# Optimization experiments

Measured on AMD Instinct MI355X. Metric: run time of the kernel, lower is better.

Reference implementation:

```python
import jax, jax.numpy as jnp
import numpy as np
import math

MAX_K = 8
MAX_LEN = 128
ITER = 3
GAMMA = 2
NEG = -2.0**16 + 1.0  # mask fill value from torch code


def _squash(x):
    # NOTE: faithful to source: norm taken over axis=1 (capsule axis), keepdim
    sq = jnp.sum(x * x, axis=1, keepdims=True)
    return sq / (1.0 + sq) / jnp.sqrt(sq + 1e-9) * x


def _routing(low, B_mat, S):
    # low: [B, n, d] mailbox; B_mat: [1, MAX_K, MAX_LEN]; S: [d, d]
    n = low.shape[1]
    K_c = max(1, min(MAX_K, int(math.log2(n))))  # static per edge type
    low_new = jnp.einsum('bnd,de->bne', low, S)  # loop-invariant in torch too
    B_c = B_mat[:, :K_c, :]
    mask = jnp.arange(MAX_LEN) < n  # padded-neighbor mask
    high = None
    for _ in range(ITER):
        logits = jnp.where(mask, B_c, NEG)              # [1,K_c,L]
        W = jax.nn.softmax(logits, axis=-1)[:, :, :n]   # weights identical over batch
        high = _squash(jnp.einsum('xkn,bnd->bkd', W, low_new))
        delta = jnp.einsum('bkd,bnd->kn', high, low_new)  # batch-summed agreement
        B_c = B_c.at[0, :, :n].add(delta)  # padded cols get zero delta (zeros in low)
    high = jnp.pad(high, ((0, 0), (0, MAX_K - K_c), (0, 0)))
    # torch B_matrix_c aliases B_matrix; write slice back so next etype sees updates
    return high, B_mat.at[:, :K_c, :].set(B_c)


def setup_inputs() -> dict:
    key = jax.random.key(0)
    ks = jax.random.split(key, 12)
    d = 64
    n_user, n_rev, n_tag, n_rev_dst = 10000, 30000, 40000, 8000
    f = lambda k, s: jax.random.normal(k, s, dtype=jnp.float32)
    return {
        'review_embed': f(ks[0], (n_rev, d)),
        'tag_embed': f(ks[1], (n_tag, d)),
        'idx_urt': jax.random.randint(ks[2], (n_user, 64), 0, n_rev, dtype=jnp.int32),
        'idx_uqt': jax.random.randint(ks[3], (n_user, 32), 0, n_tag, dtype=jnp.int32),
        'idx_uprt': jax.random.randint(ks[4], (n_user, 50), 0, n_rev, dtype=jnp.int32),
        'idx_rht': jax.random.randint(ks[5], (n_rev_dst, 20), 0, n_tag, dtype=jnp.int32),
        'B_matrix': f(ks[6], (1, MAX_K, MAX_LEN)),
        'S_matrix': f(ks[7], (d, d)),
        'M1': f(ks[8], (d, d)),
        'M2': f(ks[9], (d, 1)),
    }


def reference(review_embed, tag_embed, idx_urt, idx_uqt, idx_uprt, idx_rht,
              B_matrix, S_matrix, M1, M2):
    # capsule routing per edge type, B_matrix threaded sequentially (torch aliasing)
    h_urt, B_matrix = _routing(review_embed[idx_urt], B_matrix, S_matrix)
    h_uqt, B_matrix = _routing(tag_embed[idx_uqt], B_matrix, S_matrix)
    h_uprt, B_matrix = _routing(review_embed[idx_uprt], B_matrix, S_matrix)
    all_u = jnp.concatenate([h_urt, h_uqt, h_uprt], axis=1)  # [B, 3*MAX_K, d]
    s = jnp.einsum('bkd,do->bko', jnp.tanh(jnp.einsum('bkd,de->bke', all_u, M1)), M2)[..., 0]
    s = s ** GAMMA
    att = jax.nn.softmax(s, axis=1)                # [B, 3*MAX_K]
    user_out = jnp.einsum('bk,bkd->bd', att, all_u)
    review_out = jnp.mean(tag_embed[idx_rht], axis=1)  # flag==2 mean reduce (r_h_t)
    return user_out, review_out
```

## Files before the change

kernel.cpp:

```cpp
#include <hip/hip_runtime.h>

#define NU 10000
#define NREV_DST 8000
#define MAIN_BLOCKS 2500


__device__ __forceinline__ float rlane(float v, int l) {
    return __int_as_float(__builtin_amdgcn_readlane(__float_as_int(v), l));
}

template <int N, int K>
__global__ __launch_bounds__(256, 4) void main_iter(
    const float* __restrict__ emb, const int* __restrict__ idx,
    const float* __restrict__ Sg, const float* __restrict__ Wg,
    float* __restrict__ delta_acc, float* __restrict__ allu,
    int slot0, int write_high, int write_delta)
{
    __shared__ float s_S[64 * 64];
    __shared__ float s_embT[4][64 * 20];

    const int tid  = threadIdx.x;
    const int w    = tid >> 6;
    const int lane = tid & 63;

    for (int i = tid; i < 64 * 64; i += 256) {
        const int r = i >> 6, c = i & 63;
        s_S[r * 64 + ((((c >> 2) ^ (r & 15)) << 2) | (c & 3))] = Sg[i];
    }
    __syncthreads();

    const int u = __builtin_amdgcn_readfirstlane((int)blockIdx.x * 4 + w);
    const int* uidx = idx + u * N;

    float g[K];
#pragma unroll
    for (int k = 0; k < K; ++k) g[k] = 0.f;
#pragma unroll
    for (int r0 = 0; r0 < N; r0 += 8) {
        float ev[8];
#pragma unroll
        for (int i = 0; i < 8; ++i)
            if (r0 + i < N) {
                const int row = uidx[r0 + i];
                ev[i] = emb[(size_t)row * 64 + lane];
            }
#pragma unroll
        for (int i = 0; i < 8; ++i)
            if (r0 + i < N) {
#pragma unroll
                for (int k = 0; k < K; ++k)
                    g[k] = fmaf(Wg[(r0 + i) * 8 + k], ev[i], g[k]);
            }
    }

    float raw[K];
#pragma unroll
    for (int k = 0; k < K; ++k) raw[k] = 0.f;
    {
        const int l4 = lane >> 2, lo = lane & 3;
#pragma unroll 4
        for (int eo = 0; eo < 16; ++eo) {
            const int a = eo * 64 + (((l4 ^ eo) << 2) | lo);
            const float sv0 = s_S[a];
            const float sv1 = s_S[a + 16 * 64];
            const float sv2 = s_S[a + 32 * 64];
            const float sv3 = s_S[a + 48 * 64];
#pragma unroll
            for (int k = 0; k < K; ++k) {
                raw[k] = fmaf(rlane(g[k], eo),      sv0, raw[k]);
                raw[k] = fmaf(rlane(g[k], eo + 16), sv1, raw[k]);
                raw[k] = fmaf(rlane(g[k], eo + 32), sv2, raw[k]);
                raw[k] = fmaf(rlane(g[k], eo + 48), sv3, raw[k]);
            }
        }
    }

    float sq = 0.f;
#pragma unroll
    for (int k = 0; k < K; ++k) sq = fmaf(raw[k], raw[k], sq);
    const float f = (sq / (1.0f + sq)) / sqrtf(sq + 1e-9f);
    float hi[K];
#pragma unroll
    for (int k = 0; k < K; ++k) hi[k] = f * raw[k];

    if (write_high) {
#pragma unroll
        for (int k = 0; k < K; ++k)
            allu[(size_t)u * 1024 + (slot0 + k) * 64 + lane] = hi[k];
    }

    if (write_delta) {
        float hs[K];
#pragma unroll
        for (int k = 0; k < K; ++k) hs[k] = 0.f;
        {
            const int rowbase = lane * 64, l15 = lane & 15;
#pragma unroll 4
            for (int d4 = 0; d4 < 16; ++d4) {
                const float4 sv = *(const float4*)&s_S[rowbase + ((d4 ^ l15) << 2)];
#pragma unroll
                for (int k = 0; k < K; ++k) {
                    hs[k] = fmaf(rlane(hi[k], d4 * 4 + 0), sv.x, hs[k]);
                    hs[k] = fmaf(rlane(hi[k], d4 * 4 + 1), sv.y, hs[k]);
                    hs[k] = fmaf(rlane(hi[k], d4 * 4 + 2), sv.z, hs[k]);
                    hs[k] = fmaf(rlane(hi[k], d4 * 4 + 3), sv.w, hs[k]);
                }
            }
        }

        float dreg[K];
#pragma unroll
        for (int k = 0; k < K; ++k) dreg[k] = 0.f;

        constexpr int RP = (N + 15) / 16;
        const int rr = lane >> 2, jj = lane & 3;
        int rows[RP];
#pragma unroll
        for (int p = 0; p < RP; ++p) {
            const int r = p * 16 + rr;
            rows[p] = (N % 16 == 0 || r < N) ? uidx[r] : 0;
        }

        for (int ec = 0; ec < 4; ++ec) {
            const int e0 = ec * 16;
#pragma unroll
            for (int p = 0; p < RP; ++p) {
                const int r = p * 16 + rr;
                if (N % 16 == 0 || r < N) {
                    const float4 v =
                        *(const float4*)(emb + (size_t)rows[p] * 64 + e0 + jj * 4);
                    *(float4*)&s_embT[w][r * 20 + jj * 4] = v;
                }
            }
#pragma unroll
            for (int e4 = 0; e4 < 4; ++e4) {
                const float4 v = *(const float4*)&s_embT[w][lane * 20 + e4 * 4];
                const int e = e0 + e4 * 4;
#pragma unroll
                for (int k = 0; k < K; ++k) {
                    dreg[k] = fmaf(v.x, rlane(hs[k], e + 0), dreg[k]);
                    dreg[k] = fmaf(v.y, rlane(hs[k], e + 1), dreg[k]);
                    dreg[k] = fmaf(v.z, rlane(hs[k], e + 2), dreg[k]);
                    dreg[k] = fmaf(v.w, rlane(hs[k], e + 3), dreg[k]);
                }
            }
        }

#pragma unroll
        for (int k = 0; k < K; ++k) s_embT[w][k * 64 + lane] = dreg[k];
        __syncthreads();
        for (int t = tid; t < K * 64; t += 256) {
            const float s = s_embT[0][t] + s_embT[1][t] + s_embT[2][t] + s_embT[3][t];
            if ((t & 63) < N) atomicAdd(&delta_acc[t], s);
        }
    }
}

__global__ __launch_bounds__(1024) void update_kernel(
    float* __restrict__ Bstate, float* __restrict__ delta_acc,
    const float* __restrict__ Bin, float* __restrict__ Wout,
    int init, int Kc, int nc, int Kn, int nn)
{
    __shared__ float sB[1024];
    const int t = threadIdx.x;
    float b = init ? Bin[t] : Bstate[t];
    const int k = t >> 7, n = t & 127;
    float d = 0.f;
    if (!init && k < Kc && n < nc) d = delta_acc[k * 64 + n];
    __syncthreads();
    if (t < 512) delta_acc[t] = 0.f;
    b += d;
    Bstate[t] = b;
    sB[t] = b;
    __syncthreads();
    const int wv = t >> 6, lane = t & 63;
    if (wv < Kn) {
        float v = (lane < nn) ? sB[wv * 128 + lane] : -3.4e38f;
        float m = v;
#pragma unroll
        for (int off = 32; off >= 1; off >>= 1) m = fmaxf(m, __shfl_xor(m, off, 64));
        const float e = (lane < nn) ? expf(v - m) : 0.f;
        float s = e;
#pragma unroll
        for (int off = 32; off >= 1; off >>= 1) s += __shfl_xor(s, off, 64);
        Wout[lane * 8 + wv] = e / s;
    }
}

__global__ __launch_bounds__(256) void attn_kernel(
    const float* __restrict__ allu, const float* __restrict__ M1g,
    const float* __restrict__ M2g, float* __restrict__ out)
{
    __shared__ float sM1[64 * 65];
    __shared__ float sU[4][16 * 64];
    const int tid = threadIdx.x, w = tid >> 6, lane = tid & 63;
    for (int i = tid; i < 4096; i += 256)
        sM1[(i >> 6) * 65 + (i & 63)] = M1g[i];
    __syncthreads();
    const int u = blockIdx.x * 4 + w;
    if (u >= NU) return;
    for (int i = 0; i < 16; ++i)
        sU[w][i * 64 + lane] = allu[(size_t)u * 1024 + i * 64 + lane];
    const float m2 = M2g[lane];
    float acc[16];
#pragma unroll
    for (int i = 0; i < 16; ++i) acc[i] = 0.f;
    for (int d = 0; d < 64; ++d) {
        const float m1v = sM1[d * 65 + lane];
#pragma unroll
        for (int i = 0; i < 16; ++i) acc[i] = fmaf(sU[w][i * 64 + d], m1v, acc[i]);
    }
    float s2[16];
#pragma unroll
    for (int i = 0; i < 16; ++i) {
        float c = tanhf(acc[i]) * m2;
#pragma unroll
        for (int off = 32; off >= 1; off >>= 1) c += __shfl_xor(c, off, 64);
        s2[i] = c * c;
    }
    float mx = 0.f;
#pragma unroll
    for (int i = 0; i < 16; ++i) mx = fmaxf(mx, s2[i]);
    float den = 8.f * expf(-mx);
    float att[16];
#pragma unroll
    for (int i = 0; i < 16; ++i) { att[i] = expf(s2[i] - mx); den += att[i]; }
    const float inv = 1.0f / den;
    float o = 0.f;
#pragma unroll
    for (int i = 0; i < 16; ++i) o = fmaf(att[i] * inv, sU[w][i * 64 + lane], o);
    out[(size_t)u * 64 + lane] = o;
}

__global__ __launch_bounds__(256) void review_kernel(
    const float* __restrict__ tag, const int* __restrict__ idx, float* __restrict__ out)
{
    const int tid = threadIdx.x, w = tid >> 6, lane = tid & 63;
    const int r = blockIdx.x * 4 + w;
    if (r >= NREV_DST) return;
    float acc = 0.f;
    for (int j = 0; j < 20; ++j) {
        const int t = idx[r * 20 + j];
        acc += tag[(size_t)t * 64 + lane];
    }
    out[(size_t)r * 64 + lane] = acc / 20.0f;
}

extern "C" void kernel_launch(void* const* d_in, const int* in_sizes, int n_in,
                              void* d_out, int out_size, void* d_ws, size_t ws_size,
                              hipStream_t stream)
{
    const float* review_embed = (const float*)d_in[0];
    const float* tag_embed    = (const float*)d_in[1];
    const int*   idx_urt      = (const int*)d_in[2];
    const int*   idx_uqt      = (const int*)d_in[3];
    const int*   idx_uprt     = (const int*)d_in[4];
    const int*   idx_rht      = (const int*)d_in[5];
    const float* B_in         = (const float*)d_in[6];
    const float* S_g          = (const float*)d_in[7];
    const float* M1           = (const float*)d_in[8];
    const float* M2           = (const float*)d_in[9];

    float* ws     = (float*)d_ws;
    float* Bstate = ws;
    float* delta  = ws + 1024;
    float* Wbuf   = ws + 1536;
    float* allu   = ws + 2048;
    float* out    = (float*)d_out;

    const dim3 mg(MAIN_BLOCKS), mb(256);
    const dim3 one(1), ub(1024);

    hipLaunchKernelGGL(update_kernel, one, ub, 0, stream,
                       Bstate, delta, B_in, Wbuf, 1, 0, 0, 6, 64);

    for (int itr = 0; itr < 3; ++itr) {
        hipLaunchKernelGGL((main_iter<64, 6>), mg, mb, 0, stream,
                           review_embed, idx_urt, S_g, Wbuf, delta, allu,
                           0, (itr == 2) ? 1 : 0, 1);
        const int Kn = (itr == 2) ? 5 : 6;
        const int nn = (itr == 2) ? 32 : 64;
        hipLaunchKernelGGL(update_kernel, one, ub, 0, stream,
                           Bstate, delta, B_in, Wbuf, 0, 6, 64, Kn, nn);
    }
    for (int itr = 0; itr < 3; ++itr) {
        hipLaunchKernelGGL((main_iter<32, 5>), mg, mb, 0, stream,
                           tag_embed, idx_uqt, S_g, Wbuf, delta, allu,
                           6, (itr == 2) ? 1 : 0, 1);
        const int nn = (itr == 2) ? 50 : 32;
        hipLaunchKernelGGL(update_kernel, one, ub, 0, stream,
                           Bstate, delta, B_in, Wbuf, 0, 5, 32, 5, nn);
    }
    for (int itr = 0; itr < 3; ++itr) {
        const int last = (itr == 2);
        hipLaunchKernelGGL((main_iter<50, 5>), mg, mb, 0, stream,
                           review_embed, idx_uprt, S_g, Wbuf, delta, allu,
                           11, last, last ? 0 : 1);
        if (!last)
            hipLaunchKernelGGL(update_kernel, one, ub, 0, stream,
                               Bstate, delta, B_in, Wbuf, 0, 5, 50, 5, 50);
    }

    hipLaunchKernelGGL(attn_kernel, dim3((NU + 3) / 4), mb, 0, stream, allu, M1, M2, out);
    hipLaunchKernelGGL(review_kernel, dim3((NREV_DST + 3) / 4), mb, 0, stream,
                       tag_embed, idx_rht, out + (size_t)NU * 64);
}
```

Baseline: 793.3 us.

## Precompute embedding-times-S tables and drop in-kernel S matmuls

Adds a kernel that multiplies each embedding table by S once per edge type, so the routing kernels gather pre-transformed rows instead of applying S per user per iteration. The delta step now dots high vectors directly against the transformed rows held in shared memory, replacing the S-projection and readlane broadcasts. This removes the per-block S load into shared memory and most of the FMAs, and raises occupancy hints. In exchange it adds three table-transform launches and extra workspace traffic, and recomputes the review table twice.

```diff
diff --git a/kernel.cpp b/kernel.cpp
--- a/kernel.cpp
+++ b/kernel.cpp
@@ -5,36 +5,46 @@
 #define MAIN_BLOCKS 2500
 
 
-__device__ __forceinline__ float rlane(float v, int l) {
-    return __int_as_float(__builtin_amdgcn_readlane(__float_as_int(v), l));
+__global__ __launch_bounds__(256) void embS_kernel(
+    const float* __restrict__ E, const float* __restrict__ Sg,
+    float* __restrict__ out, int nrows)
+{
+    const int tid = threadIdx.x, w = tid >> 6, lane = tid & 63;
+    float Sc[64];
+#pragma unroll
+    for (int e = 0; e < 64; ++e) Sc[e] = Sg[e * 64 + lane];
+    const int nw = gridDim.x * 4;
+    for (int r0 = blockIdx.x * 4 + w; r0 < nrows; r0 += nw) {
+        const int r = __builtin_amdgcn_readfirstlane(r0);
+        const float* row = E + (size_t)r * 64;
+        float acc = 0.f;
+#pragma unroll
+        for (int e = 0; e < 64; ++e)
+            acc = fmaf(row[e], Sc[e], acc);
+        out[(size_t)r * 64 + lane] = acc;
+    }
 }
 
 template <int N, int K>
-__global__ __launch_bounds__(256, 4) void main_iter(
-    const float* __restrict__ emb, const int* __restrict__ idx,
-    const float* __restrict__ Sg, const float* __restrict__ Wg,
+__global__ __launch_bounds__(256, 6) void main_iter(
+    const float* __restrict__ embS, const int* __restrict__ idx,
+    const float* __restrict__ Wg,
     float* __restrict__ delta_acc, float* __restrict__ allu,
     int slot0, int write_high, int write_delta)
 {
-    __shared__ float s_S[64 * 64];
-    __shared__ float s_embT[4][64 * 20];
+    __shared__ float s_slab[4][64 * 20];
+    __shared__ float s_h[4][K * 64];
 
     const int tid  = threadIdx.x;
     const int w    = tid >> 6;
     const int lane = tid & 63;
 
-    for (int i = tid; i < 64 * 64; i += 256) {
-        const int r = i >> 6, c = i & 63;
-        s_S[r * 64 + ((((c >> 2) ^ (r & 15)) << 2) | (c & 3))] = Sg[i];
-    }
-    __syncthreads();
-
     const int u = __builtin_amdgcn_readfirstlane((int)blockIdx.x * 4 + w);
     const int* uidx = idx + u * N;
 
-    float g[K];
-#pragma unroll
-    for (int k = 0; k < K; ++k) g[k] = 0.f;
+    float raw[K];
+#pragma unroll
+    for (int k = 0; k < K; ++k) raw[k] = 0.f;
 #pragma unroll
     for (int r0 = 0; r0 < N; r0 += 8) {
         float ev[8];
@@ -42,37 +52,15 @@
         for (int i = 0; i < 8; ++i)
             if (r0 + i < N) {
                 const int row = uidx[r0 + i];
-                ev[i] = emb[(size_t)row * 64 + lane];
+                ev[i] = embS[(size_t)row * 64 + lane];
             }
 #pragma unroll
         for (int i = 0; i < 8; ++i)
             if (r0 + i < N) {
 #pragma unroll
                 for (int k = 0; k < K; ++k)
-                    g[k] = fmaf(Wg[(r0 + i) * 8 + k], ev[i], g[k]);
-            }
-    }
-
-    float raw[K];
-#pragma unroll
-    for (int k = 0; k < K; ++k) raw[k] = 0.f;
-    {
-        const int l4 = lane >> 2, lo = lane & 3;
-#pragma unroll 4
-        for (int eo = 0; eo < 16; ++eo) {
-            const int a = eo * 64 + (((l4 ^ eo) << 2) | lo);
-            const float sv0 = s_S[a];
-            const float sv1 = s_S[a + 16 * 64];
-            const float sv2 = s_S[a + 32 * 64];
-            const float sv3 = s_S[a + 48 * 64];
-#pragma unroll
-            for (int k = 0; k < K; ++k) {
-                raw[k] = fmaf(rlane(g[k], eo),      sv0, raw[k]);
-                raw[k] = fmaf(rlane(g[k], eo + 16), sv1, raw[k]);
-                raw[k] = fmaf(rlane(g[k], eo + 32), sv2, raw[k]);
-                raw[k] = fmaf(rlane(g[k], eo + 48), sv3, raw[k]);
-            }
-        }
+                    raw[k] = fmaf(Wg[(r0 + i) * 8 + k], ev[i], raw[k]);
+            }
     }
 
     float sq = 0.f;
@@ -90,23 +78,8 @@
     }
 
     if (write_delta) {
-        float hs[K];
-#pragma unroll
-        for (int k = 0; k < K; ++k) hs[k] = 0.f;
-        {
-            const int rowbase = lane * 64, l15 = lane & 15;
-#pragma unroll 4
-            for (int d4 = 0; d4 < 16; ++d4) {
-                const float4 sv = *(const float4*)&s_S[rowbase + ((d4 ^ l15) << 2)];
-#pragma unroll
-                for (int k = 0; k < K; ++k) {
-                    hs[k] = fmaf(rlane(hi[k], d4 * 4 + 0), sv.x, hs[k]);
-                    hs[k] = fmaf(rlane(hi[k], d4 * 4 + 1), sv.y, hs[k]);
-                    hs[k] = fmaf(rlane(hi[k], d4 * 4 + 2), sv.z, hs[k]);
-                    hs[k] = fmaf(rlane(hi[k], d4 * 4 + 3), sv.w, hs[k]);
-                }
-            }
-        }
+#pragma unroll
+        for (int k = 0; k < K; ++k) s_h[w][k * 64 + lane] = hi[k];
 
         float dreg[K];
 #pragma unroll
@@ -128,29 +101,29 @@
                 const int r = p * 16 + rr;
                 if (N % 16 == 0 || r < N) {
                     const float4 v =
-                        *(const float4*)(emb + (size_t)rows[p] * 64 + e0 + jj * 4);
-                    *(float4*)&s_embT[w][r * 20 + jj * 4] = v;
+                        *(const float4*)(embS + (size_t)rows[p] * 64 + e0 + jj * 4);
+                    *(float4*)&s_slab[w][r * 20 + jj * 4] = v;
                 }
             }
 #pragma unroll
             for (int e4 = 0; e4 < 4; ++e4) {
-                const float4 v = *(const float4*)&s_embT[w][lane * 20 + e4 * 4];
-                const int e = e0 + e4 * 4;
+                const float4 v = *(const float4*)&s_slab[w][lane * 20 + e4 * 4];
 #pragma unroll
                 for (int k = 0; k < K; ++k) {
-                    dreg[k] = fmaf(v.x, rlane(hs[k], e + 0), dreg[k]);
-                    dreg[k] = fmaf(v.y, rlane(hs[k], e + 1), dreg[k]);
-                    dreg[k] = fmaf(v.z, rlane(hs[k], e + 2), dreg[k]);
-                    dreg[k] = fmaf(v.w, rlane(hs[k], e + 3), dreg[k]);
+                    const float4 h = *(const float4*)&s_h[w][k * 64 + e0 + e4 * 4];
+                    dreg[k] = fmaf(v.x, h.x, dreg[k]);
+                    dreg[k] = fmaf(v.y, h.y, dreg[k]);
+                    dreg[k] = fmaf(v.z, h.z, dreg[k]);
+                    dreg[k] = fmaf(v.w, h.w, dreg[k]);
                 }
             }
         }
 
 #pragma unroll
-        for (int k = 0; k < K; ++k) s_embT[w][k * 64 + lane] = dreg[k];
+        for (int k = 0; k < K; ++k) s_slab[w][k * 64 + lane] = dreg[k];
         __syncthreads();
         for (int t = tid; t < K * 64; t += 256) {
-            const float s = s_embT[0][t] + s_embT[1][t] + s_embT[2][t] + s_embT[3][t];
+            const float s = s_slab[0][t] + s_slab[1][t] + s_slab[2][t] + s_slab[3][t];
             if ((t & 63) < N) atomicAdd(&delta_acc[t], s);
         }
     }
@@ -266,35 +239,41 @@
     float* delta  = ws + 1024;
     float* Wbuf   = ws + 1536;
     float* allu   = ws + 2048;
+    float* embS   = ws + 2048 + (size_t)NU * 1024;
     float* out    = (float*)d_out;
 
     const dim3 mg(MAIN_BLOCKS), mb(256);
-    const dim3 one(1), ub(1024);
-
+    const dim3 one(1), ub(1024), pg(512);
+
+    hipLaunchKernelGGL(embS_kernel, pg, mb, 0, stream, review_embed, S_g, embS, 30000);
     hipLaunchKernelGGL(update_kernel, one, ub, 0, stream,
                        Bstate, delta, B_in, Wbuf, 1, 0, 0, 6, 64);
 
     for (int itr = 0; itr < 3; ++itr) {
         hipLaunchKernelGGL((main_iter<64, 6>), mg, mb, 0, stream,
-                           review_embed, idx_urt, S_g, Wbuf, delta, allu,
+                           embS, idx_urt, Wbuf, delta, allu,
                            0, (itr == 2) ? 1 : 0, 1);
         const int Kn = (itr == 2) ? 5 : 6;
         const int nn = (itr == 2) ? 32 : 64;
         hipLaunchKernelGGL(update_kernel, one, ub, 0, stream,
                            Bstate, delta, B_in, Wbuf, 0, 6, 64, Kn, nn);
     }
+
+    hipLaunchKernelGGL(embS_kernel, pg, mb, 0, stream, tag_embed, S_g, embS, 40000);
     for (int itr = 0; itr < 3; ++itr) {
         hipLaunchKernelGGL((main_iter<32, 5>), mg, mb, 0, stream,
-                           tag_embed, idx_uqt, S_g, Wbuf, delta, allu,
+                           embS, idx_uqt, Wbuf, delta, allu,
                            6, (itr == 2) ? 1 : 0, 1);
         const int nn = (itr == 2) ? 50 : 32;
         hipLaunchKernelGGL(update_kernel, one, ub, 0, stream,
                            Bstate, delta, B_in, Wbuf, 0, 5, 32, 5, nn);
     }
+
+    hipLaunchKernelGGL(embS_kernel, pg, mb, 0, stream, review_embed, S_g, embS, 30000);
     for (int itr = 0; itr < 3; ++itr) {
         const int last = (itr == 2);
         hipLaunchKernelGGL((main_iter<50, 5>), mg, mb, 0, stream,
-                           review_embed, idx_uprt, S_g, Wbuf, delta, allu,
+                           embS, idx_uprt, Wbuf, delta, allu,
                            11, last, last ? 0 : 1);
         if (!last)
             hipLaunchKernelGGL(update_kernel, one, ub, 0, stream,
```

Result: slower. 1.134 ms (+42.9%).

## Replace readlane broadcasts with LDS-staged vectors and fuse init with review kernel

Applied to the files above, without the earlier changes.

The S-matrix products and the delta reduction no longer broadcast per-wave vectors with scalar readlane instructions. Each wave now stages its g, hi and hs vectors in shared memory and reads them back as float4 broadcasts, with a simpler XOR swizzle on S. The embedding slab for the delta step shrinks to 8-column chunks, and the gather loop is unrolled to 16 rows. The initial B/softmax setup is merged with the review mean kernel into one launch, removing a kernel launch. The cost is more LDS traffic and an extra block-wide barrier.

```diff
diff --git a/kernel.cpp b/kernel.cpp
--- a/kernel.cpp
+++ b/kernel.cpp
@@ -4,10 +4,6 @@
 #define NREV_DST 8000
 #define MAIN_BLOCKS 2500
 
-
-__device__ __forceinline__ float rlane(float v, int l) {
-    return __int_as_float(__builtin_amdgcn_readlane(__float_as_int(v), l));
-}
 
 template <int N, int K>
 __global__ __launch_bounds__(256, 4) void main_iter(
@@ -17,7 +13,9 @@
     int slot0, int write_high, int write_delta)
 {
     __shared__ float s_S[64 * 64];
-    __shared__ float s_embT[4][64 * 20];
+    __shared__ float s_slab[4][64 * 10];
+    __shared__ float s_g[4][K * 64];
+    __shared__ float s_h[4][K * 64];
 
     const int tid  = threadIdx.x;
     const int w    = tid >> 6;
@@ -25,7 +23,7 @@
 
     for (int i = tid; i < 64 * 64; i += 256) {
         const int r = i >> 6, c = i & 63;
-        s_S[r * 64 + ((((c >> 2) ^ (r & 15)) << 2) | (c & 3))] = Sg[i];
+        s_S[r * 64 + (c ^ ((r & 15) << 2))] = Sg[i];
     }
     __syncthreads();
 
@@ -36,16 +34,16 @@
 #pragma unroll
     for (int k = 0; k < K; ++k) g[k] = 0.f;
 #pragma unroll
-    for (int r0 = 0; r0 < N; r0 += 8) {
-        float ev[8];
-#pragma unroll
-        for (int i = 0; i < 8; ++i)
+    for (int r0 = 0; r0 < N; r0 += 16) {
+        float ev[16];
+#pragma unroll
+        for (int i = 0; i < 16; ++i)
             if (r0 + i < N) {
                 const int row = uidx[r0 + i];
                 ev[i] = emb[(size_t)row * 64 + lane];
             }
 #pragma unroll
-        for (int i = 0; i < 8; ++i)
+        for (int i = 0; i < 16; ++i)
             if (r0 + i < N) {
 #pragma unroll
                 for (int k = 0; k < K; ++k)
@@ -53,25 +51,26 @@
             }
     }
 
+#pragma unroll
+    for (int k = 0; k < K; ++k) s_g[w][k * 64 + lane] = g[k];
     float raw[K];
 #pragma unroll
     for (int k = 0; k < K; ++k) raw[k] = 0.f;
-    {
-        const int l4 = lane >> 2, lo = lane & 3;
-#pragma unroll 4
-        for (int eo = 0; eo < 16; ++eo) {
-            const int a = eo * 64 + (((l4 ^ eo) << 2) | lo);
-            const float sv0 = s_S[a];
-            const float sv1 = s_S[a + 16 * 64];
-            const float sv2 = s_S[a + 32 * 64];
-            const float sv3 = s_S[a + 48 * 64];
-#pragma unroll
-            for (int k = 0; k < K; ++k) {
-                raw[k] = fmaf(rlane(g[k], eo),      sv0, raw[k]);
-                raw[k] = fmaf(rlane(g[k], eo + 16), sv1, raw[k]);
-                raw[k] = fmaf(rlane(g[k], eo + 32), sv2, raw[k]);
-                raw[k] = fmaf(rlane(g[k], eo + 48), sv3, raw[k]);
-            }
+#pragma unroll
+    for (int e0 = 0; e0 < 64; e0 += 4) {
+        float sv[4];
+#pragma unroll
+        for (int j = 0; j < 4; ++j) {
+            const int e = e0 + j;
+            sv[j] = s_S[e * 64 + (lane ^ ((e & 15) << 2))];
+        }
+#pragma unroll
+        for (int k = 0; k < K; ++k) {
+            const float4 g4 = *(const float4*)&s_g[w][k * 64 + e0];
+            raw[k] = fmaf(g4.x, sv[0], raw[k]);
+            raw[k] = fmaf(g4.y, sv[1], raw[k]);
+            raw[k] = fmaf(g4.z, sv[2], raw[k]);
+            raw[k] = fmaf(g4.w, sv[3], raw[k]);
         }
     }
 
@@ -90,23 +89,25 @@
     }
 
     if (write_delta) {
+#pragma unroll
+        for (int k = 0; k < K; ++k) s_h[w][k * 64 + lane] = hi[k];
         float hs[K];
 #pragma unroll
         for (int k = 0; k < K; ++k) hs[k] = 0.f;
-        {
-            const int rowbase = lane * 64, l15 = lane & 15;
-#pragma unroll 4
-            for (int d4 = 0; d4 < 16; ++d4) {
-                const float4 sv = *(const float4*)&s_S[rowbase + ((d4 ^ l15) << 2)];
-#pragma unroll
-                for (int k = 0; k < K; ++k) {
-                    hs[k] = fmaf(rlane(hi[k], d4 * 4 + 0), sv.x, hs[k]);
-                    hs[k] = fmaf(rlane(hi[k], d4 * 4 + 1), sv.y, hs[k]);
-                    hs[k] = fmaf(rlane(hi[k], d4 * 4 + 2), sv.z, hs[k]);
-                    hs[k] = fmaf(rlane(hi[k], d4 * 4 + 3), sv.w, hs[k]);
-                }
-            }
-        }
+#pragma unroll
+        for (int c4 = 0; c4 < 16; ++c4) {
+            const float4 sv = *(const float4*)&s_S[lane * 64 + ((c4 ^ (lane & 15)) << 2)];
+#pragma unroll
+            for (int k = 0; k < K; ++k) {
+                const float4 h4 = *(const float4*)&s_h[w][k * 64 + c4 * 4];
+                hs[k] = fmaf(h4.x, sv.x, hs[k]);
+                hs[k] = fmaf(h4.y, sv.y, hs[k]);
+                hs[k] = fmaf(h4.z, sv.z, hs[k]);
+                hs[k] = fmaf(h4.w, sv.w, hs[k]);
+            }
+        }
+#pragma unroll
+        for (int k = 0; k < K; ++k) s_g[w][k * 64 + lane] = hs[k];
 
         float dreg[K];
 #pragma unroll
@@ -121,36 +122,42 @@
             rows[p] = (N % 16 == 0 || r < N) ? uidx[r] : 0;
         }
 
-        for (int ec = 0; ec < 4; ++ec) {
-            const int e0 = ec * 16;
+        for (int ec = 0; ec < 8; ++ec) {
+            const int e0 = ec * 8;
 #pragma unroll
             for (int p = 0; p < RP; ++p) {
                 const int r = p * 16 + rr;
                 if (N % 16 == 0 || r < N) {
-                    const float4 v =
-                        *(const float4*)(emb + (size_t)rows[p] * 64 + e0 + jj * 4);
-                    *(float4*)&s_embT[w][r * 20 + jj * 4] = v;
+                    const float2 v =
+                        *(const float2*)(emb + (size_t)rows[p] * 64 + e0 + jj * 2);
+                    *(float2*)&s_slab[w][r * 10 + jj * 2] = v;
                 }
             }
-#pragma unroll
-            for (int e4 = 0; e4 < 4; ++e4) {
-                const float4 v = *(const float4*)&s_embT[w][lane * 20 + e4 * 4];
-                const int e = e0 + e4 * 4;
-#pragma unroll
-                for (int k = 0; k < K; ++k) {
-                    dreg[k] = fmaf(v.x, rlane(hs[k], e + 0), dreg[k]);
-                    dreg[k] = fmaf(v.y, rlane(hs[k], e + 1), dreg[k]);
-                    dreg[k] = fmaf(v.z, rlane(hs[k], e + 2), dreg[k]);
-                    dreg[k] = fmaf(v.w, rlane(hs[k], e + 3), dreg[k]);
-                }
-            }
-        }
-
-#pragma unroll
-        for (int k = 0; k < K; ++k) s_embT[w][k * 64 + lane] = dreg[k];
+            const float2 v0 = *(const float2*)&s_slab[w][lane * 10 + 0];
+            const float2 v1 = *(const float2*)&s_slab[w][lane * 10 + 2];
+            const float2 v2 = *(const float2*)&s_slab[w][lane * 10 + 4];
+            const float2 v3 = *(const float2*)&s_slab[w][lane * 10 + 6];
+#pragma unroll
+            for (int k = 0; k < K; ++k) {
+                const float4 hA = *(const float4*)&s_g[w][k * 64 + e0];
+                const float4 hB = *(const float4*)&s_g[w][k * 64 + e0 + 4];
+                dreg[k] = fmaf(v0.x, hA.x, dreg[k]);
+                dreg[k] = fmaf(v0.y, hA.y, dreg[k]);
+                dreg[k] = fmaf(v1.x, hA.z, dreg[k]);
+                dreg[k] = fmaf(v1.y, hA.w, dreg[k]);
+                dreg[k] = fmaf(v2.x, hB.x, dreg[k]);
+                dreg[k] = fmaf(v2.y, hB.y, dreg[k]);
+                dreg[k] = fmaf(v3.x, hB.z, dreg[k]);
+                dreg[k] = fmaf(v3.y, hB.w, dreg[k]);
+            }
+        }
+
+        __syncthreads();
+#pragma unroll
+        for (int k = 0; k < K; ++k) s_slab[w][k * 64 + lane] = dreg[k];
         __syncthreads();
         for (int t = tid; t < K * 64; t += 256) {
-            const float s = s_embT[0][t] + s_embT[1][t] + s_embT[2][t] + s_embT[3][t];
+            const float s = s_slab[0][t] + s_slab[1][t] + s_slab[2][t] + s_slab[3][t];
             if ((t & 63) < N) atomicAdd(&delta_acc[t], s);
         }
     }
@@ -187,6 +194,41 @@
     }
 }
 
+__global__ __launch_bounds__(256) void init_review_kernel(
+    float* __restrict__ ws, const float* __restrict__ Bin,
+    const float* __restrict__ tag, const int* __restrict__ idx,
+    float* __restrict__ rout)
+{
+    const int t = threadIdx.x, w = t >> 6, lane = t & 63;
+    if (blockIdx.x == 0) {
+        __shared__ float sB[1024];
+        for (int i = t; i < 1024; i += 256) { const float b = Bin[i]; ws[i] = b; sB[i] = b; }
+        for (int i = t; i < 512; i += 256) ws[1024 + i] = 0.f;
+        __syncthreads();
+#pragma unroll
+        for (int wv = w; wv < 6; wv += 4) {
+            float v = sB[wv * 128 + lane];
+            float m = v;
+#pragma unroll
+            for (int off = 32; off >= 1; off >>= 1) m = fmaxf(m, __shfl_xor(m, off, 64));
+            const float e = expf(v - m);
+            float s = e;
+#pragma unroll
+            for (int off = 32; off >= 1; off >>= 1) s += __shfl_xor(s, off, 64);
+            ws[1536 + lane * 8 + wv] = e / s;
+        }
+        return;
+    }
+    const int r = (blockIdx.x - 1) * 4 + w;
+    if (r >= NREV_DST) return;
+    float acc = 0.f;
+    for (int j = 0; j < 20; ++j) {
+        const int tg = idx[r * 20 + j];
+        acc += tag[(size_t)tg * 64 + lane];
+    }
+    rout[(size_t)r * 64 + lane] = acc / 20.0f;
+}
+
 __global__ __launch_bounds__(256) void attn_kernel(
     const float* __restrict__ allu, const float* __restrict__ M1g,
     const float* __restrict__ M2g, float* __restrict__ out)
@@ -232,20 +274,6 @@
     out[(size_t)u * 64 + lane] = o;
 }
 
-__global__ __launch_bounds__(256) void review_kernel(
-    const float* __restrict__ tag, const int* __restrict__ idx, float* __restrict__ out)
-{
-    const int tid = threadIdx.x, w = tid >> 6, lane = tid & 63;
-    const int r = blockIdx.x * 4 + w;
-    if (r >= NREV_DST) return;
-    float acc = 0.f;
-    for (int j = 0; j < 20; ++j) {
-        const int t = idx[r * 20 + j];
-        acc += tag[(size_t)t * 64 + lane];
-    }
-    out[(size_t)r * 64 + lane] = acc / 20.0f;
-}
-
 extern "C" void kernel_launch(void* const* d_in, const int* in_sizes, int n_in,
                               void* d_out, int out_size, void* d_ws, size_t ws_size,
                               hipStream_t stream)
@@ -271,8 +299,8 @@
     const dim3 mg(MAIN_BLOCKS), mb(256);
     const dim3 one(1), ub(1024);
 
-    hipLaunchKernelGGL(update_kernel, one, ub, 0, stream,
-                       Bstate, delta, B_in, Wbuf, 1, 0, 0, 6, 64);
+    hipLaunchKernelGGL(init_review_kernel, dim3(1 + (NREV_DST + 3) / 4), mb, 0, stream,
+                       ws, B_in, tag_embed, idx_rht, out + (size_t)NU * 64);
 
     for (int itr = 0; itr < 3; ++itr) {
         hipLaunchKernelGGL((main_iter<64, 6>), mg, mb, 0, stream,
@@ -302,6 +330,4 @@
     }
 
     hipLaunchKernelGGL(attn_kernel, dim3((NU + 3) / 4), mb, 0, stream, allu, M1, M2, out);
-    hipLaunchKernelGGL(review_kernel, dim3((NREV_DST + 3) / 4), mb, 0, stream,
-                       tag_embed, idx_rht, out + (size_t)NU * 64);
-}
+}
```

After: 1.173 ms. 47.8% more time.
